# Kernel optimization log

Measured on AMD Instinct MI355X. Metric: run time of the kernel, lower is better.

The kernel has to match this reference:

```python
import jax, jax.numpy as jnp
import numpy as np


def setup_inputs() -> dict:
    key = jax.random.key(0)
    ks = jax.random.split(key, 10)
    B, T, E = 4096, 200, 64
    H0, H1, H2 = 80, 40, 1
    D = 4 * E  # concat feature dim = 256
    glorot = lambda k, shp: jax.random.normal(k, shp, jnp.float32) * jnp.sqrt(2.0 / (shp[0] + shp[1]))
    return {
        "queries": jax.random.normal(ks[0], (B, 1, E), jnp.float32),
        "keys": jax.random.normal(ks[1], (B, T, E), jnp.float32),
        "keys_length": jax.random.randint(ks[2], (B, 1), 0, T, jnp.int32),
        "W0": glorot(ks[3], (D, H0)),
        "b0": jnp.zeros((H0,), jnp.float32),
        "W1": glorot(ks[4], (H0, H1)),
        "b1": jnp.zeros((H1,), jnp.float32),
        "W2": glorot(ks[5], (H1, H2)),
        "b2": jnp.zeros((H2,), jnp.float32),
    }


def reference(queries, keys, keys_length, W0, b0, W1, b1, W2, b2):
    B, T, E = keys.shape
    # repeat query along history axis: [B,1,E] -> [B,T,E]
    q = jnp.broadcast_to(queries, (B, T, E))
    # DIN attention input: [B,T,4E]
    att = jnp.concatenate([q, keys, q - keys, q * keys], axis=-1)
    # tiny 3-layer MLP, sigmoid activations (att_activation, no output_activation override)
    h = jax.nn.sigmoid(att @ W0 + b0)
    h = jax.nn.sigmoid(h @ W1 + b1)
    score = jax.nn.sigmoid(h @ W2 + b2)          # [B,T,1]
    out = jnp.transpose(score, (0, 2, 1))         # [B,1,T]
    # sequence mask: [B,1,T]
    key_masks = jnp.arange(T)[None, None, :] < keys_length[:, :, None]
    # weight_normalization=False -> masked positions become 0, no softmax
    out = jnp.where(key_masks, out, jnp.zeros_like(out))
    # weighted sum over history: [B,1,T] @ [B,T,E] -> [B,1,E]
    return jnp.matmul(out, keys)
```

## Files before the change

kernel.cpp:

```cpp
#include <hip/hip_runtime.h>

#define NT 512
#define NWAVE 8
#define PE 136
#define PW1 104
#define PH 104

typedef __attribute__((ext_vector_type(8))) short short8;
typedef __attribute__((ext_vector_type(4))) float f32x4;

__device__ __forceinline__ unsigned short f2b(float f) {
  unsigned int x = __float_as_uint(f);
  return (unsigned short)((x + 0x7fffu + ((x >> 16) & 1u)) >> 16);
}
__device__ __forceinline__ float sigmoidf(float x) {
  return __builtin_amdgcn_rcpf(1.0f + __expf(-x));
}
__device__ __forceinline__ short8 pack8(float4 a, float4 b) {
  short8 r;
  r[0] = (short)f2b(a.x); r[1] = (short)f2b(a.y); r[2] = (short)f2b(a.z); r[3] = (short)f2b(a.w);
  r[4] = (short)f2b(b.x); r[5] = (short)f2b(b.y); r[6] = (short)f2b(b.z); r[7] = (short)f2b(b.w);
  return r;
}
__device__ __forceinline__ short8 pack8q(float4 a, float4 b, float4 qa, float4 qb) {
  short8 r;
  r[0] = (short)f2b(a.x * qa.x); r[1] = (short)f2b(a.y * qa.y);
  r[2] = (short)f2b(a.z * qa.z); r[3] = (short)f2b(a.w * qa.w);
  r[4] = (short)f2b(b.x * qb.x); r[5] = (short)f2b(b.y * qb.y);
  r[6] = (short)f2b(b.z * qb.z); r[7] = (short)f2b(b.w * qb.w);
  return r;
}

__global__ __launch_bounds__(256, 2) void prep_c(
    const float* __restrict__ q, const float* __restrict__ W0,
    const float* __restrict__ b0, float* __restrict__ C, int B)
{
  __shared__ float Wac[64 * 80];
  __shared__ float qlds[32 * 64];
  const int bbase = blockIdx.x * 32, tid = threadIdx.x;
  for (int idx = tid; idx < 5120; idx += 256) {
    const int e = idx / 80, h = idx - e * 80;
    Wac[idx] = W0[e * 80 + h] + W0[(128 + e) * 80 + h];
  }
  for (int idx = tid; idx < 2048; idx += 256) {
    const int bl = idx >> 6, e = idx & 63;
    const int bg = bbase + bl;
    qlds[idx] = (bg < B) ? q[bg * 64 + e] : 0.0f;
  }
  __syncthreads();
  #pragma unroll
  for (int i = 0; i < 10; ++i) {
    const int idx = tid + i * 256;
    const int bl = idx / 80, h = idx - bl * 80;
    const int bg = bbase + bl;
    if (bg < B) {
      float acc = b0[h];
      #pragma unroll 8
      for (int e = 0; e < 64; ++e) acc += qlds[bl * 64 + e] * Wac[e * 80 + h];
      C[bg * 80 + h] = acc;
    }
  }
}

__global__ __launch_bounds__(NT, 2) void din_attn_main(
    const float* __restrict__ q,
    const float* __restrict__ keys,
    const int* __restrict__ klen,
    const float* __restrict__ W0,
    const float* __restrict__ b0,
    const float* __restrict__ W1,
    const float* __restrict__ b1,
    const float* __restrict__ W2,
    const float* __restrict__ b2,
    float* __restrict__ out,
    const float* __restrict__ Cpre,
    int B)
{
  __shared__ __align__(16) unsigned short WxT[80 * PE];
  __shared__ __align__(16) unsigned short W1T[48 * PW1];
  __shared__ __align__(16) unsigned short h0s[NWAVE][16 * PH];

  const int tid = threadIdx.x;

  for (int idx = tid; idx < 128 * 80; idx += NT) {
    const int e = idx / 80, h = idx - e * 80;
    const float v = (e < 64)
        ? (W0[(64 + e) * 80 + h] - W0[(128 + e) * 80 + h])
        : W0[(128 + e) * 80 + h];
    WxT[h * PE + e] = f2b(v);
  }
  for (int idx = tid; idx < 48 * PW1; idx += NT) {
    const int j = idx / PW1, h = idx - j * PW1;
    W1T[idx] = (j < 40 && h < 80) ? f2b(W1[h * 40 + j]) : (unsigned short)0;
  }
  {
    const int w0i = tid >> 6, ln = tid & 63;
    for (int i = ln; i < 256; i += 64)
      h0s[w0i][(i >> 4) * PH + 80 + (i & 15)] = 0;
  }
  __syncthreads();

  const int wv = __builtin_amdgcn_readfirstlane(tid >> 6);
  const int lane = tid & 63;
  const int lm = lane & 15;
  const int quad = lane >> 4;
  const int b = blockIdx.x * NWAVE + wv;
  if (b >= B) return;

  int L = klen[b];
  L = __builtin_amdgcn_readfirstlane(max(0, min(200, L)));
  unsigned short* h0 = h0s[wv];

  const float* qb = q + (size_t)b * 64;
  const float4* q4 = (const float4*)qb;
  const float4 q0 = q4[quad * 2],     q1 = q4[quad * 2 + 1];
  const float4 q2 = q4[8 + quad * 2], q3 = q4[8 + quad * 2 + 1];

  float cfv[5];
  if (Cpre != nullptr) {
    #pragma unroll
    for (int nt = 0; nt < 5; ++nt) cfv[nt] = Cpre[b * 80 + nt * 16 + lm];
  } else {
    #pragma unroll
    for (int nt = 0; nt < 5; ++nt) cfv[nt] = b0[nt * 16 + lm];
    for (int e = 0; e < 64; ++e) {
      const float qv = qb[e];
      #pragma unroll
      for (int nt = 0; nt < 5; ++nt) {
        const int col = nt * 16 + lm;
        cfv[nt] += qv * (W0[e * 80 + col] + W0[(128 + e) * 80 + col]);
      }
    }
  }
  float b1v[3], w2v[3];
  #pragma unroll
  for (int nt = 0; nt < 3; ++nt) {
    const int col = nt * 16 + lm;
    b1v[nt] = (col < 40) ? b1[col] : 0.0f;
    w2v[nt] = (col < 40) ? W2[col] : 0.0f;
  }
  const float b2v = b2[0];

  const float* kb = keys + (size_t)b * 12800;
  float wacc = 0.0f;
  const int ntile = (L + 15) >> 4;

  const float4 z4 = {0.0f, 0.0f, 0.0f, 0.0f};
  float4 k0 = z4, k1 = z4, k2 = z4, k3 = z4;
  if (ntile > 0 && lm < L) {
    const float4* kp = (const float4*)(kb + (size_t)lm * 64);
    k0 = kp[quad * 2]; k1 = kp[quad * 2 + 1];
    k2 = kp[8 + quad * 2]; k3 = kp[8 + quad * 2 + 1];
  }

  for (int p = 0; p < ntile; ++p) {
    const short8 a0  = pack8(k0, k1);
    const short8 a1  = pack8(k2, k3);
    const short8 aq0 = pack8q(k0, k1, q0, q1);
    const short8 aq1 = pack8q(k2, k3, q2, q3);

    if (p + 1 < ntile) {
      const int t = ((p + 1) << 4) + lm;
      if (t < L) {
        const float4* kp = (const float4*)(kb + (size_t)t * 64);
        k0 = kp[quad * 2]; k1 = kp[quad * 2 + 1];
        k2 = kp[8 + quad * 2]; k3 = kp[8 + quad * 2 + 1];
      } else { k0 = k1 = k2 = k3 = z4; }
    }

    #pragma unroll
    for (int nt = 0; nt < 5; ++nt) {
      const int col = nt * 16 + lm;
      const unsigned short* wr = &WxT[col * PE + quad * 8];
      const short8 w0 = *(const short8*)(wr);
      const short8 w1 = *(const short8*)(wr + 32);
      const short8 w2 = *(const short8*)(wr + 64);
      const short8 w3 = *(const short8*)(wr + 96);
      f32x4 acc;
      acc[0] = cfv[nt]; acc[1] = cfv[nt]; acc[2] = cfv[nt]; acc[3] = cfv[nt];
      acc = __builtin_amdgcn_mfma_f32_16x16x32_bf16(a0,  w0, acc, 0, 0, 0);
      acc = __builtin_amdgcn_mfma_f32_16x16x32_bf16(a1,  w1, acc, 0, 0, 0);
      acc = __builtin_amdgcn_mfma_f32_16x16x32_bf16(aq0, w2, acc, 0, 0, 0);
      acc = __builtin_amdgcn_mfma_f32_16x16x32_bf16(aq1, w3, acc, 0, 0, 0);
      #pragma unroll
      for (int r = 0; r < 4; ++r)
        h0[(quad * 4 + r) * PH + col] = f2b(sigmoidf(acc[r]));
    }

    const short8 ha0 = *(const short8*)&h0[lm * PH + quad * 8];
    const short8 ha1 = *(const short8*)&h0[lm * PH + 32 + quad * 8];
    const short8 ha2 = *(const short8*)&h0[lm * PH + 64 + quad * 8];
    float pd[4] = {0.0f, 0.0f, 0.0f, 0.0f};
    #pragma unroll
    for (int nt = 0; nt < 3; ++nt) {
      const int col = nt * 16 + lm;
      const unsigned short* wr = &W1T[col * PW1 + quad * 8];
      const short8 wb0 = *(const short8*)(wr);
      const short8 wb1 = *(const short8*)(wr + 32);
      const short8 wb2 = *(const short8*)(wr + 64);
      f32x4 acc;
      acc[0] = b1v[nt]; acc[1] = b1v[nt]; acc[2] = b1v[nt]; acc[3] = b1v[nt];
      acc = __builtin_amdgcn_mfma_f32_16x16x32_bf16(ha0, wb0, acc, 0, 0, 0);
      acc = __builtin_amdgcn_mfma_f32_16x16x32_bf16(ha1, wb1, acc, 0, 0, 0);
      acc = __builtin_amdgcn_mfma_f32_16x16x32_bf16(ha2, wb2, acc, 0, 0, 0);
      #pragma unroll
      for (int r = 0; r < 4; ++r) pd[r] += sigmoidf(acc[r]) * w2v[nt];
    }
    #pragma unroll
    for (int r = 0; r < 4; ++r) {
      pd[r] += __shfl_xor(pd[r], 1);
      pd[r] += __shfl_xor(pd[r], 2);
      pd[r] += __shfl_xor(pd[r], 4);
      pd[r] += __shfl_xor(pd[r], 8);
    }
    float sc[4];
    #pragma unroll
    for (int r = 0; r < 4; ++r) sc[r] = sigmoidf(pd[r] + b2v);

    const int t0 = p << 4;
    const int nr = min(16, L - t0);
    const float* krow = kb + (size_t)t0 * 64 + lane;
    #pragma unroll
    for (int t = 0; t < 16; ++t) {
      if (t < nr) {
        const float sv = __shfl(sc[t & 3], ((t >> 2) << 4) + lm);
        wacc += sv * krow[(size_t)t * 64];
      }
    }
  }

  out[(size_t)b * 64 + lane] = wacc;
}

extern "C" void kernel_launch(void* const* d_in, const int* in_sizes, int n_in,
                              void* d_out, int out_size, void* d_ws, size_t ws_size,
                              hipStream_t stream) {
  const int B = in_sizes[2];
  const float* Cpre = nullptr;
  if (ws_size >= (size_t)B * 80 * sizeof(float)) {
    float* C = (float*)d_ws;
    prep_c<<<(B + 31) / 32, 256, 0, stream>>>(
        (const float*)d_in[0], (const float*)d_in[3], (const float*)d_in[4], C, B);
    Cpre = C;
  }
  din_attn_main<<<(B + NWAVE - 1) / NWAVE, NT, 0, stream>>>(
      (const float*)d_in[0], (const float*)d_in[1], (const int*)d_in[2],
      (const float*)d_in[3], (const float*)d_in[4], (const float*)d_in[5],
      (const float*)d_in[6], (const float*)d_in[7], (const float*)d_in[8],
      (float*)d_out, Cpre, B);
}
```

Baseline: 370.9 us.

## Split sequences into 32-step units with atomic work-stealing across waves

Work is no longer one wave per batch row. Each row's history is split into 32-timestep units, and units are handed out through per-cluster atomic counters, so waves in a 64-row cluster balance the uneven key lengths dynamically. Each unit processes two 16-row MFMA tiles and accumulates its weighted-key partial sum into the output with atomicAdd, which requires zeroing the output and counters with memsets. The hidden-layer padding is trimmed so the third K-slice is loaded only by two quads. The cost is extra atomics, memset launches, and reloading q and C once per unit.

```diff
diff --git a/kernel.cpp b/kernel.cpp
--- a/kernel.cpp
+++ b/kernel.cpp
@@ -3,8 +3,11 @@
 #define NT 512
 #define NWAVE 8
 #define PE 136
-#define PW1 104
-#define PH 104
+#define PW1 88
+#define PH 88
+#define UPB 7
+#define BPC 64
+#define SPC (BPC * UPB)
 
 typedef __attribute__((ext_vector_type(8))) short short8;
 typedef __attribute__((ext_vector_type(4))) float f32x4;
@@ -74,11 +77,13 @@
     const float* __restrict__ b2,
     float* __restrict__ out,
     const float* __restrict__ Cpre,
+    unsigned int* __restrict__ ctrs,
     int B)
 {
   __shared__ __align__(16) unsigned short WxT[80 * PE];
   __shared__ __align__(16) unsigned short W1T[48 * PW1];
-  __shared__ __align__(16) unsigned short h0s[NWAVE][16 * PH];
+  __shared__ __align__(16) unsigned short h0s[NWAVE][32 * PH];
+  __shared__ __align__(16) float scb[NWAVE][32];
 
   const int tid = threadIdx.x;
 
@@ -93,45 +98,16 @@
     const int j = idx / PW1, h = idx - j * PW1;
     W1T[idx] = (j < 40 && h < 80) ? f2b(W1[h * 40 + j]) : (unsigned short)0;
   }
-  {
-    const int w0i = tid >> 6, ln = tid & 63;
-    for (int i = ln; i < 256; i += 64)
-      h0s[w0i][(i >> 4) * PH + 80 + (i & 15)] = 0;
-  }
   __syncthreads();
 
   const int wv = __builtin_amdgcn_readfirstlane(tid >> 6);
   const int lane = tid & 63;
   const int lm = lane & 15;
   const int quad = lane >> 4;
-  const int b = blockIdx.x * NWAVE + wv;
-  if (b >= B) return;
-
-  int L = klen[b];
-  L = __builtin_amdgcn_readfirstlane(max(0, min(200, L)));
+  const int gw = blockIdx.x * NWAVE + wv;
   unsigned short* h0 = h0s[wv];
-
-  const float* qb = q + (size_t)b * 64;
-  const float4* q4 = (const float4*)qb;
-  const float4 q0 = q4[quad * 2],     q1 = q4[quad * 2 + 1];
-  const float4 q2 = q4[8 + quad * 2], q3 = q4[8 + quad * 2 + 1];
-
-  float cfv[5];
-  if (Cpre != nullptr) {
-    #pragma unroll
-    for (int nt = 0; nt < 5; ++nt) cfv[nt] = Cpre[b * 80 + nt * 16 + lm];
-  } else {
-    #pragma unroll
-    for (int nt = 0; nt < 5; ++nt) cfv[nt] = b0[nt * 16 + lm];
-    for (int e = 0; e < 64; ++e) {
-      const float qv = qb[e];
-      #pragma unroll
-      for (int nt = 0; nt < 5; ++nt) {
-        const int col = nt * 16 + lm;
-        cfv[nt] += qv * (W0[e * 80 + col] + W0[(128 + e) * 80 + col]);
-      }
-    }
-  }
+  float* scl = scb[wv];
+
   float b1v[3], w2v[3];
   #pragma unroll
   for (int nt = 0; nt < 3; ++nt) {
@@ -140,32 +116,57 @@
     w2v[nt] = (col < 40) ? W2[col] : 0.0f;
   }
   const float b2v = b2[0];
-
-  const float* kb = keys + (size_t)b * 12800;
-  float wacc = 0.0f;
-  const int ntile = (L + 15) >> 4;
-
+  const short8 z8 = {0, 0, 0, 0, 0, 0, 0, 0};
   const float4 z4 = {0.0f, 0.0f, 0.0f, 0.0f};
-  float4 k0 = z4, k1 = z4, k2 = z4, k3 = z4;
-  if (ntile > 0 && lm < L) {
-    const float4* kp = (const float4*)(kb + (size_t)lm * 64);
-    k0 = kp[quad * 2]; k1 = kp[quad * 2 + 1];
-    k2 = kp[8 + quad * 2]; k3 = kp[8 + quad * 2 + 1];
-  }
-
-  for (int p = 0; p < ntile; ++p) {
-    const short8 a0  = pack8(k0, k1);
-    const short8 a1  = pack8(k2, k3);
-    const short8 aq0 = pack8q(k0, k1, q0, q1);
-    const short8 aq1 = pack8q(k2, k3, q2, q3);
-
-    if (p + 1 < ntile) {
-      const int t = ((p + 1) << 4) + lm;
+
+  auto unit = [&](int b, int u, int L) {
+    const float4* q4 = (const float4*)(q + (size_t)b * 64);
+    const float4 q0 = q4[quad * 2],     q1 = q4[quad * 2 + 1];
+    const float4 q2 = q4[8 + quad * 2], q3 = q4[8 + quad * 2 + 1];
+
+    float cfv[5];
+    if (Cpre != nullptr) {
+      #pragma unroll
+      for (int nt = 0; nt < 5; ++nt) cfv[nt] = Cpre[b * 80 + nt * 16 + lm];
+    } else {
+      #pragma unroll
+      for (int nt = 0; nt < 5; ++nt) cfv[nt] = b0[nt * 16 + lm];
+      for (int e = 0; e < 64; ++e) {
+        const float qv = q[(size_t)b * 64 + e];
+        #pragma unroll
+        for (int nt = 0; nt < 5; ++nt)
+          cfv[nt] += qv * (W0[e * 80 + nt * 16 + lm] + W0[(128 + e) * 80 + nt * 16 + lm]);
+      }
+    }
+
+    const float* kb = keys + (size_t)b * 12800;
+    const int t0 = u << 5;
+    const int nr = min(32, L - t0);
+    const bool two = nr > 16;
+
+    short8 a0, a1, aq0, aq1;
+    {
+      const int t = t0 + lm;
+      float4 k0 = z4, k1 = z4, k2 = z4, k3 = z4;
       if (t < L) {
         const float4* kp = (const float4*)(kb + (size_t)t * 64);
         k0 = kp[quad * 2]; k1 = kp[quad * 2 + 1];
         k2 = kp[8 + quad * 2]; k3 = kp[8 + quad * 2 + 1];
-      } else { k0 = k1 = k2 = k3 = z4; }
+      }
+      a0 = pack8(k0, k1); a1 = pack8(k2, k3);
+      aq0 = pack8q(k0, k1, q0, q1); aq1 = pack8q(k2, k3, q2, q3);
+    }
+    short8 c0 = z8, c1 = z8, cq0 = z8, cq1 = z8;
+    if (two) {
+      const int t = t0 + 16 + lm;
+      float4 k0 = z4, k1 = z4, k2 = z4, k3 = z4;
+      if (t < L) {
+        const float4* kp = (const float4*)(kb + (size_t)t * 64);
+        k0 = kp[quad * 2]; k1 = kp[quad * 2 + 1];
+        k2 = kp[8 + quad * 2]; k3 = kp[8 + quad * 2 + 1];
+      }
+      c0 = pack8(k0, k1); c1 = pack8(k2, k3);
+      cq0 = pack8q(k0, k1, q0, q1); cq1 = pack8q(k2, k3, q2, q3);
     }
 
     #pragma unroll
@@ -185,67 +186,151 @@
       #pragma unroll
       for (int r = 0; r < 4; ++r)
         h0[(quad * 4 + r) * PH + col] = f2b(sigmoidf(acc[r]));
-    }
-
-    const short8 ha0 = *(const short8*)&h0[lm * PH + quad * 8];
-    const short8 ha1 = *(const short8*)&h0[lm * PH + 32 + quad * 8];
-    const short8 ha2 = *(const short8*)&h0[lm * PH + 64 + quad * 8];
-    float pd[4] = {0.0f, 0.0f, 0.0f, 0.0f};
+      if (two) {
+        f32x4 ac2;
+        ac2[0] = cfv[nt]; ac2[1] = cfv[nt]; ac2[2] = cfv[nt]; ac2[3] = cfv[nt];
+        ac2 = __builtin_amdgcn_mfma_f32_16x16x32_bf16(c0,  w0, ac2, 0, 0, 0);
+        ac2 = __builtin_amdgcn_mfma_f32_16x16x32_bf16(c1,  w1, ac2, 0, 0, 0);
+        ac2 = __builtin_amdgcn_mfma_f32_16x16x32_bf16(cq0, w2, ac2, 0, 0, 0);
+        ac2 = __builtin_amdgcn_mfma_f32_16x16x32_bf16(cq1, w3, ac2, 0, 0, 0);
+        #pragma unroll
+        for (int r = 0; r < 4; ++r)
+          h0[(16 + quad * 4 + r) * PH + col] = f2b(sigmoidf(ac2[r]));
+      }
+    }
+
+    const short8 ha00 = *(const short8*)&h0[lm * PH + quad * 8];
+    const short8 ha01 = *(const short8*)&h0[lm * PH + 32 + quad * 8];
+    short8 ha02 = z8;
+    if (quad < 2) ha02 = *(const short8*)&h0[lm * PH + 64 + quad * 8];
+    short8 ha10 = z8, ha11 = z8, ha12 = z8;
+    if (two) {
+      ha10 = *(const short8*)&h0[(16 + lm) * PH + quad * 8];
+      ha11 = *(const short8*)&h0[(16 + lm) * PH + 32 + quad * 8];
+      if (quad < 2) ha12 = *(const short8*)&h0[(16 + lm) * PH + 64 + quad * 8];
+    }
+    float pd0[4] = {0, 0, 0, 0}, pd1[4] = {0, 0, 0, 0};
     #pragma unroll
     for (int nt = 0; nt < 3; ++nt) {
       const int col = nt * 16 + lm;
       const unsigned short* wr = &W1T[col * PW1 + quad * 8];
       const short8 wb0 = *(const short8*)(wr);
       const short8 wb1 = *(const short8*)(wr + 32);
-      const short8 wb2 = *(const short8*)(wr + 64);
+      short8 wb2 = z8;
+      if (quad < 2) wb2 = *(const short8*)(wr + 64);
       f32x4 acc;
       acc[0] = b1v[nt]; acc[1] = b1v[nt]; acc[2] = b1v[nt]; acc[3] = b1v[nt];
-      acc = __builtin_amdgcn_mfma_f32_16x16x32_bf16(ha0, wb0, acc, 0, 0, 0);
-      acc = __builtin_amdgcn_mfma_f32_16x16x32_bf16(ha1, wb1, acc, 0, 0, 0);
-      acc = __builtin_amdgcn_mfma_f32_16x16x32_bf16(ha2, wb2, acc, 0, 0, 0);
-      #pragma unroll
-      for (int r = 0; r < 4; ++r) pd[r] += sigmoidf(acc[r]) * w2v[nt];
+      acc = __builtin_amdgcn_mfma_f32_16x16x32_bf16(ha00, wb0, acc, 0, 0, 0);
+      acc = __builtin_amdgcn_mfma_f32_16x16x32_bf16(ha01, wb1, acc, 0, 0, 0);
+      acc = __builtin_amdgcn_mfma_f32_16x16x32_bf16(ha02, wb2, acc, 0, 0, 0);
+      #pragma unroll
+      for (int r = 0; r < 4; ++r) pd0[r] += sigmoidf(acc[r]) * w2v[nt];
+      if (two) {
+        f32x4 ac2;
+        ac2[0] = b1v[nt]; ac2[1] = b1v[nt]; ac2[2] = b1v[nt]; ac2[3] = b1v[nt];
+        ac2 = __builtin_amdgcn_mfma_f32_16x16x32_bf16(ha10, wb0, ac2, 0, 0, 0);
+        ac2 = __builtin_amdgcn_mfma_f32_16x16x32_bf16(ha11, wb1, ac2, 0, 0, 0);
+        ac2 = __builtin_amdgcn_mfma_f32_16x16x32_bf16(ha12, wb2, ac2, 0, 0, 0);
+        #pragma unroll
+        for (int r = 0; r < 4; ++r) pd1[r] += sigmoidf(ac2[r]) * w2v[nt];
+      }
     }
     #pragma unroll
     for (int r = 0; r < 4; ++r) {
-      pd[r] += __shfl_xor(pd[r], 1);
-      pd[r] += __shfl_xor(pd[r], 2);
-      pd[r] += __shfl_xor(pd[r], 4);
-      pd[r] += __shfl_xor(pd[r], 8);
-    }
-    float sc[4];
-    #pragma unroll
-    for (int r = 0; r < 4; ++r) sc[r] = sigmoidf(pd[r] + b2v);
-
-    const int t0 = p << 4;
-    const int nr = min(16, L - t0);
-    const float* krow = kb + (size_t)t0 * 64 + lane;
-    #pragma unroll
-    for (int t = 0; t < 16; ++t) {
+      pd0[r] += __shfl_xor(pd0[r], 1);
+      pd0[r] += __shfl_xor(pd0[r], 2);
+      pd0[r] += __shfl_xor(pd0[r], 4);
+      pd0[r] += __shfl_xor(pd0[r], 8);
+    }
+    if (two) {
+      #pragma unroll
+      for (int r = 0; r < 4; ++r) {
+        pd1[r] += __shfl_xor(pd1[r], 1);
+        pd1[r] += __shfl_xor(pd1[r], 2);
+        pd1[r] += __shfl_xor(pd1[r], 4);
+        pd1[r] += __shfl_xor(pd1[r], 8);
+      }
+    }
+    if (lm == 0) {
+      #pragma unroll
+      for (int r = 0; r < 4; ++r) scl[quad * 4 + r] = sigmoidf(pd0[r] + b2v);
+      if (two) {
+        #pragma unroll
+        for (int r = 0; r < 4; ++r) scl[16 + quad * 4 + r] = sigmoidf(pd1[r] + b2v);
+      }
+    }
+    float4 sv[8];
+    #pragma unroll
+    for (int i = 0; i < 8; ++i) sv[i] = *(const float4*)&scl[i * 4];
+
+    const float* kcol = kb + (size_t)t0 * 64 + lane;
+    float wacc = 0.0f;
+    #pragma unroll
+    for (int t = 0; t < 32; ++t) {
       if (t < nr) {
-        const float sv = __shfl(sc[t & 3], ((t >> 2) << 4) + lm);
-        wacc += sv * krow[(size_t)t * 64];
-      }
-    }
-  }
-
-  out[(size_t)b * 64 + lane] = wacc;
+        const int i = t >> 2, j = t & 3;
+        const float s = (j == 0) ? sv[i].x : (j == 1) ? sv[i].y : (j == 2) ? sv[i].z : sv[i].w;
+        wacc += s * kcol[(size_t)t * 64];
+      }
+    }
+    atomicAdd(&out[(size_t)b * 64 + lane], wacc);
+  };
+
+  if (ctrs != nullptr) {
+    const int c = gw >> 6;
+    unsigned int* ctr = ctrs + (size_t)c * 32;
+    unsigned int v0 = 0u;
+    if (lane == 0) v0 = atomicAdd(ctr, 1u);
+    int s = (int)__builtin_amdgcn_readfirstlane(v0);
+    while (s < SPC) {
+      unsigned int vn = 0u;
+      if (lane == 0) vn = atomicAdd(ctr, 1u);
+      const int b = (c << 6) + (s & 63);
+      const int u = s >> 6;
+      if (b < B) {
+        int L = klen[b];
+        L = __builtin_amdgcn_readfirstlane(max(0, min(200, L)));
+        if (u * 32 < L) unit(b, u, L);
+      }
+      s = (int)__builtin_amdgcn_readfirstlane(vn);
+    }
+  } else {
+    const int b = gw;
+    if (b < B) {
+      int L = klen[b];
+      L = __builtin_amdgcn_readfirstlane(max(0, min(200, L)));
+      for (int u = 0; u * 32 < L; ++u) unit(b, u, L);
+    }
+  }
 }
 
 extern "C" void kernel_launch(void* const* d_in, const int* in_sizes, int n_in,
                               void* d_out, int out_size, void* d_ws, size_t ws_size,
                               hipStream_t stream) {
   const int B = in_sizes[2];
+  const size_t csize = (size_t)B * 80 * sizeof(float);
+  const int nctr = (B + BPC - 1) / BPC;
+  const size_t ctrbytes = (size_t)nctr * 32 * sizeof(unsigned int);
+
   const float* Cpre = nullptr;
-  if (ws_size >= (size_t)B * 80 * sizeof(float)) {
-    float* C = (float*)d_ws;
+  unsigned int* ctrs = nullptr;
+  size_t off = 0;
+  if (ws_size >= csize) { Cpre = (const float*)d_ws; off = csize; }
+  off = (off + 127) & ~(size_t)127;
+  if (ws_size >= off + ctrbytes) {
+    ctrs = (unsigned int*)((char*)d_ws + off);
+    hipMemsetAsync(ctrs, 0, ctrbytes, stream);
+  }
+  hipMemsetAsync(d_out, 0, (size_t)out_size, stream);
+
+  if (Cpre != nullptr) {
     prep_c<<<(B + 31) / 32, 256, 0, stream>>>(
-        (const float*)d_in[0], (const float*)d_in[3], (const float*)d_in[4], C, B);
-    Cpre = C;
+        (const float*)d_in[0], (const float*)d_in[3], (const float*)d_in[4],
+        (float*)d_ws, B);
   }
   din_attn_main<<<(B + NWAVE - 1) / NWAVE, NT, 0, stream>>>(
       (const float*)d_in[0], (const float*)d_in[1], (const int*)d_in[2],
       (const float*)d_in[3], (const float*)d_in[4], (const float*)d_in[5],
       (const float*)d_in[6], (const float*)d_in[7], (const float*)d_in[8],
-      (float*)d_out, Cpre, B);
-}
+      (float*)d_out, Cpre, ctrs, B);
+}
```

Measured after the change: 370.7 us. No clear change (-0.1%).

## Restructure weighted-sum to per-lane float4 rows, use DPP reductions and setprio

Applied to the files above, without the earlier changes.

The per-tile weighted sum over keys changes. It no longer does 16 serialized shuffles with scalar loads per lane. Each lane now loads float4 key rows matching its MFMA output rows, accumulates a float4 partial, and reduces across quads once after the loop. The 16-lane score reduction uses DPP row operations instead of ds_swizzle shuffles, q is pre-packed to bf16 once, and s_setprio brackets the MFMA sections. This removes per-tile shuffle latency. In exchange it adds extra vector loads, and bf16-rounded q slightly changes the q*k precision.

```diff
diff --git a/kernel.cpp b/kernel.cpp
--- a/kernel.cpp
+++ b/kernel.cpp
@@ -9,9 +9,16 @@
 typedef __attribute__((ext_vector_type(8))) short short8;
 typedef __attribute__((ext_vector_type(4))) float f32x4;
 
+#define DPP_ADD(x, ctrl)                                                    \
+  ((x) + __uint_as_float(__builtin_amdgcn_mov_dpp(                          \
+             __float_as_uint(x), (ctrl), 0xf, 0xf, true)))
+
 __device__ __forceinline__ unsigned short f2b(float f) {
   unsigned int x = __float_as_uint(f);
   return (unsigned short)((x + 0x7fffu + ((x >> 16) & 1u)) >> 16);
+}
+__device__ __forceinline__ float b2f(unsigned short u) {
+  return __uint_as_float(((unsigned int)u) << 16);
 }
 __device__ __forceinline__ float sigmoidf(float x) {
   return __builtin_amdgcn_rcpf(1.0f + __expf(-x));
@@ -22,12 +29,16 @@
   r[4] = (short)f2b(b.x); r[5] = (short)f2b(b.y); r[6] = (short)f2b(b.z); r[7] = (short)f2b(b.w);
   return r;
 }
-__device__ __forceinline__ short8 pack8q(float4 a, float4 b, float4 qa, float4 qb) {
+__device__ __forceinline__ short8 pack8qb(float4 a, float4 b, short8 qp) {
   short8 r;
-  r[0] = (short)f2b(a.x * qa.x); r[1] = (short)f2b(a.y * qa.y);
-  r[2] = (short)f2b(a.z * qa.z); r[3] = (short)f2b(a.w * qa.w);
-  r[4] = (short)f2b(b.x * qb.x); r[5] = (short)f2b(b.y * qb.y);
-  r[6] = (short)f2b(b.z * qb.z); r[7] = (short)f2b(b.w * qb.w);
+  r[0] = (short)f2b(a.x * b2f((unsigned short)qp[0]));
+  r[1] = (short)f2b(a.y * b2f((unsigned short)qp[1]));
+  r[2] = (short)f2b(a.z * b2f((unsigned short)qp[2]));
+  r[3] = (short)f2b(a.w * b2f((unsigned short)qp[3]));
+  r[4] = (short)f2b(b.x * b2f((unsigned short)qp[4]));
+  r[5] = (short)f2b(b.y * b2f((unsigned short)qp[5]));
+  r[6] = (short)f2b(b.z * b2f((unsigned short)qp[6]));
+  r[7] = (short)f2b(b.w * b2f((unsigned short)qp[7]));
   return r;
 }
 
@@ -111,10 +122,9 @@
   L = __builtin_amdgcn_readfirstlane(max(0, min(200, L)));
   unsigned short* h0 = h0s[wv];
 
-  const float* qb = q + (size_t)b * 64;
-  const float4* q4 = (const float4*)qb;
-  const float4 q0 = q4[quad * 2],     q1 = q4[quad * 2 + 1];
-  const float4 q2 = q4[8 + quad * 2], q3 = q4[8 + quad * 2 + 1];
+  const float4* q4 = (const float4*)(q + (size_t)b * 64);
+  const short8 qpk0 = pack8(q4[quad * 2], q4[quad * 2 + 1]);
+  const short8 qpk1 = pack8(q4[8 + quad * 2], q4[8 + quad * 2 + 1]);
 
   float cfv[5];
   if (Cpre != nullptr) {
@@ -124,7 +134,7 @@
     #pragma unroll
     for (int nt = 0; nt < 5; ++nt) cfv[nt] = b0[nt * 16 + lm];
     for (int e = 0; e < 64; ++e) {
-      const float qv = qb[e];
+      const float qv = q[(size_t)b * 64 + e];
       #pragma unroll
       for (int nt = 0; nt < 5; ++nt) {
         const int col = nt * 16 + lm;
@@ -140,34 +150,42 @@
     w2v[nt] = (col < 40) ? W2[col] : 0.0f;
   }
   const float b2v = b2[0];
+  const short8 z8 = {0, 0, 0, 0, 0, 0, 0, 0};
+  const float4 z4 = {0.0f, 0.0f, 0.0f, 0.0f};
 
   const float* kb = keys + (size_t)b * 12800;
-  float wacc = 0.0f;
-  const int ntile = (L + 15) >> 4;
-
-  const float4 z4 = {0.0f, 0.0f, 0.0f, 0.0f};
+  float4 w4 = {0.0f, 0.0f, 0.0f, 0.0f};
+  const int passes = (L + 15) >> 4;
+
   float4 k0 = z4, k1 = z4, k2 = z4, k3 = z4;
-  if (ntile > 0 && lm < L) {
+  if (passes > 0 && lm < L) {
     const float4* kp = (const float4*)(kb + (size_t)lm * 64);
     k0 = kp[quad * 2]; k1 = kp[quad * 2 + 1];
     k2 = kp[8 + quad * 2]; k3 = kp[8 + quad * 2 + 1];
   }
 
-  for (int p = 0; p < ntile; ++p) {
-    const short8 a0  = pack8(k0, k1);
-    const short8 a1  = pack8(k2, k3);
-    const short8 aq0 = pack8q(k0, k1, q0, q1);
-    const short8 aq1 = pack8q(k2, k3, q2, q3);
-
-    if (p + 1 < ntile) {
-      const int t = ((p + 1) << 4) + lm;
+  for (int p = 0; p < passes; ++p) {
+    const int t0 = p << 4;
+
+    short8 a0 = pack8(k0, k1), a1 = pack8(k2, k3);
+    short8 aq0 = pack8qb(k0, k1, qpk0), aq1 = pack8qb(k2, k3, qpk1);
+    if (!((t0 + lm) < L)) { a0 = z8; a1 = z8; aq0 = z8; aq1 = z8; }
+
+    float4 kv[4];
+    #pragma unroll
+    for (int r = 0; r < 4; ++r)
+      kv[r] = *(const float4*)(kb + (size_t)min(t0 + 4 * quad + r, 199) * 64 + 4 * lm);
+
+    if (p + 1 < passes) {
+      const int t = t0 + 16 + lm;
       if (t < L) {
         const float4* kp = (const float4*)(kb + (size_t)t * 64);
         k0 = kp[quad * 2]; k1 = kp[quad * 2 + 1];
         k2 = kp[8 + quad * 2]; k3 = kp[8 + quad * 2 + 1];
-      } else { k0 = k1 = k2 = k3 = z4; }
-    }
-
+      } else { k0 = z4; k1 = z4; k2 = z4; k3 = z4; }
+    }
+
+    __builtin_amdgcn_s_setprio(1);
     #pragma unroll
     for (int nt = 0; nt < 5; ++nt) {
       const int col = nt * 16 + lm;
@@ -186,11 +204,13 @@
       for (int r = 0; r < 4; ++r)
         h0[(quad * 4 + r) * PH + col] = f2b(sigmoidf(acc[r]));
     }
+    __builtin_amdgcn_s_setprio(0);
 
     const short8 ha0 = *(const short8*)&h0[lm * PH + quad * 8];
     const short8 ha1 = *(const short8*)&h0[lm * PH + 32 + quad * 8];
     const short8 ha2 = *(const short8*)&h0[lm * PH + 64 + quad * 8];
     float pd[4] = {0.0f, 0.0f, 0.0f, 0.0f};
+    __builtin_amdgcn_s_setprio(1);
     #pragma unroll
     for (int nt = 0; nt < 3; ++nt) {
       const int col = nt * 16 + lm;
@@ -206,30 +226,35 @@
       #pragma unroll
       for (int r = 0; r < 4; ++r) pd[r] += sigmoidf(acc[r]) * w2v[nt];
     }
+    __builtin_amdgcn_s_setprio(0);
+
     #pragma unroll
     for (int r = 0; r < 4; ++r) {
-      pd[r] += __shfl_xor(pd[r], 1);
-      pd[r] += __shfl_xor(pd[r], 2);
-      pd[r] += __shfl_xor(pd[r], 4);
-      pd[r] += __shfl_xor(pd[r], 8);
+      pd[r] = DPP_ADD(pd[r], 0xB1);
+      pd[r] = DPP_ADD(pd[r], 0x4E);
+      pd[r] = DPP_ADD(pd[r], 0x141);
+      pd[r] = DPP_ADD(pd[r], 0x140);
     }
     float sc[4];
     #pragma unroll
-    for (int r = 0; r < 4; ++r) sc[r] = sigmoidf(pd[r] + b2v);
-
-    const int t0 = p << 4;
-    const int nr = min(16, L - t0);
-    const float* krow = kb + (size_t)t0 * 64 + lane;
-    #pragma unroll
-    for (int t = 0; t < 16; ++t) {
-      if (t < nr) {
-        const float sv = __shfl(sc[t & 3], ((t >> 2) << 4) + lm);
-        wacc += sv * krow[(size_t)t * 64];
-      }
-    }
-  }
-
-  out[(size_t)b * 64 + lane] = wacc;
+    for (int r = 0; r < 4; ++r) {
+      const int ta = t0 + 4 * quad + r;
+      sc[r] = (ta < L) ? sigmoidf(pd[r] + b2v) : 0.0f;
+    }
+
+    #pragma unroll
+    for (int r = 0; r < 4; ++r) {
+      w4.x += sc[r] * kv[r].x; w4.y += sc[r] * kv[r].y;
+      w4.z += sc[r] * kv[r].z; w4.w += sc[r] * kv[r].w;
+    }
+  }
+
+  w4.x += __shfl_xor(w4.x, 16); w4.y += __shfl_xor(w4.y, 16);
+  w4.z += __shfl_xor(w4.z, 16); w4.w += __shfl_xor(w4.w, 16);
+  w4.x += __shfl_xor(w4.x, 32); w4.y += __shfl_xor(w4.y, 32);
+  w4.z += __shfl_xor(w4.z, 32); w4.w += __shfl_xor(w4.w, 32);
+  if (lane < 16)
+    *(float4*)(out + (size_t)b * 64 + 4 * lm) = w4;
 }
 
 extern "C" void kernel_launch(void* const* d_in, const int* in_sizes, int n_in,
```

After: 320.3 us. 13.6% less time.
